# Optimization experiments

Measured on AMD Instinct MI355X. Metric: run time of the kernel, lower is better.

Reference implementation:

```python
import jax, jax.numpy as jnp
import numpy as np

BATCH = 8192
FEATURES = 8192
INITIAL_SPARSITY_RATE = 0.5


def setup_inputs() -> dict:
    key = jax.random.key(0)
    k1, _ = jax.random.split(key)
    inputs = jax.random.normal(k1, (BATCH, FEATURES), dtype=jnp.float32)
    # trainable scalar weight, shape (1,), constant-initialized
    sparsity_rate = jnp.full((1,), INITIAL_SPARSITY_RATE, dtype=jnp.float32)
    return {"inputs": inputs, "sparsity_rate": sparsity_rate}


def reference(inputs, sparsity_rate):
    # inputs: [B, F]; sparsity_rate: [1]
    n = inputs.shape[-1]
    # descending sort along feature axis
    sorted_desc = -jnp.sort(-inputs, axis=-1)
    # per-call threshold index (integer cast, non-differentiable like TF's tf.cast)
    rate = jnp.clip(sparsity_rate[0], 0.0, 1.0)
    idx = jax.lax.stop_gradient((rate * jnp.float32(n)).astype(jnp.int32))
    thresh = jnp.take(sorted_desc, idx, axis=-1)           # [B]: value at rank `idx`
    max_in = jnp.max(inputs, axis=-1)                      # [B]
    t_r = max_in - thresh                                  # [B]
    # relu-masked weights: relu(x + t_r - max) == relu(x - thresh)
    w_t = jax.nn.relu(inputs + t_r[:, None] - max_in[:, None])
    weighted_exp = w_t * jnp.exp(inputs)                   # [B, F]
    sum_we = jnp.sum(weighted_exp, axis=-1, keepdims=True)
    return weighted_exp / sum_we
```

## Files before the change

### kernel.cpp

```cpp
#include <hip/hip_runtime.h>

#define ROWS 8192
#define COLS 8192
#define TPB  256
#define EPT  32
#define VPT  8
#define NW   4

__device__ __forceinline__ unsigned f2k(float x) {
    unsigned u = __float_as_uint(x);
    return (u & 0x80000000u) ? ~u : (u | 0x80000000u);
}
__device__ __forceinline__ float k2f(unsigned k) {
    unsigned u = (k & 0x80000000u) ? (k & 0x7FFFFFFFu) : ~k;
    return __uint_as_float(u);
}

__global__ __launch_bounds__(TPB, 4)
void rsoftmax_kernel(const float* __restrict__ in,
                     const float* __restrict__ rate_p,
                     float* __restrict__ out)
{
    const int t    = threadIdx.x;
    const int lane = t & 63;
    const int wave = t >> 6;
    const int row  = blockIdx.x;
    const float4* in4  = (const float4*)(in  + (size_t)row * COLS);
    float4*       out4 = (float4*)      (out + (size_t)row * COLS);

    unsigned key[EPT];
    #pragma unroll
    for (int j = 0; j < VPT; ++j) {
        float4 v = in4[t + j * TPB];
        key[4*j+0] = f2k(v.x);
        key[4*j+1] = f2k(v.y);
        key[4*j+2] = f2k(v.z);
        key[4*j+3] = f2k(v.w);
    }

    float rate = rate_p[0];
    rate = fminf(fmaxf(rate, 0.0f), 1.0f);
    int idx = (int)(rate * (float)COLS);
    if (idx > COLS - 1) idx = COLS - 1;
    if (idx < 0) idx = 0;

    __shared__ unsigned sHistW[NW][256];
    __shared__ unsigned sWaveTot[NW];
    __shared__ unsigned sK, sPfx;
    __shared__ float    sSum[NW];
    __shared__ float    sInv;

    if (t == 0) { sK = (unsigned)(idx + 1); sPfx = 0u; }

    #pragma unroll
    for (int pass = 0; pass < 4; ++pass) {
        const int      s      = 24 - 8 * pass;
        const unsigned himask = (pass == 0) ? 0u : (0xFFFFFFFFu << (s + 8));

        __syncthreads();
        const unsigned pfx = sPfx;
        const unsigned kk  = sK;

        #pragma unroll
        for (int i = 0; i < 4; ++i) sHistW[wave][lane + 64*i] = 0u;

        #pragma unroll
        for (int j = 0; j < EPT; ++j) {
            if (((key[j] ^ pfx) & himask) == 0u)
                atomicAdd(&sHistW[wave][(key[j] >> s) & 0xFFu], 1u);
        }
        __syncthreads();

        const unsigned h = sHistW[0][t] + sHistW[1][t] + sHistW[2][t] + sHistW[3][t];

        unsigned v = h;
        #pragma unroll
        for (int off = 1; off < 64; off <<= 1) {
            unsigned u = __shfl_down(v, off, 64);
            v += (lane + off < 64) ? u : 0u;
        }
        if (lane == 0) sWaveTot[wave] = v;
        __syncthreads();

        unsigned above = 0u;
        #pragma unroll
        for (int w = 0; w < NW; ++w)
            if (w > wave) above += sWaveTot[w];

        const unsigned st = v + above;
        const unsigned sn = st - h;
        if (st >= kk && sn < kk) {
            sPfx = pfx | ((unsigned)t << s);
            sK   = kk - sn;
        }
    }
    __syncthreads();
    const float thr = k2f(sPfx);

    float wx[EPT];
    float lsum = 0.0f;
    #pragma unroll
    for (int j = 0; j < EPT; ++j) {
        float x = k2f(key[j]);
        float e = fmaxf(x - thr, 0.0f) * __expf(x);
        wx[j] = e;
        lsum += e;
    }
    #pragma unroll
    for (int off = 32; off > 0; off >>= 1)
        lsum += __shfl_down(lsum, off, 64);
    if (lane == 0) sSum[wave] = lsum;
    __syncthreads();
    if (t == 0) sInv = 1.0f / (sSum[0] + sSum[1] + sSum[2] + sSum[3]);
    __syncthreads();
    const float inv = sInv;

    #pragma unroll
    for (int j = 0; j < VPT; ++j) {
        float4 o;
        o.x = wx[4*j+0] * inv;
        o.y = wx[4*j+1] * inv;
        o.z = wx[4*j+2] * inv;
        o.w = wx[4*j+3] * inv;
        out4[t + j * TPB] = o;
    }
}

extern "C" void kernel_launch(void* const* d_in, const int* in_sizes, int n_in,
                              void* d_out, int out_size, void* d_ws, size_t ws_size,
                              hipStream_t stream)
{
    const float* in   = (const float*)d_in[0];
    const float* rate = (const float*)d_in[1];
    float*       out  = (float*)d_out;
    rsoftmax_kernel<<<dim3(ROWS), dim3(TPB), 0, stream>>>(in, rate, out);
}
```

Baseline: 457.4 us.

## Use 512-thread blocks, halve per-thread registers, recompute exp instead of storing

The block doubles to 512 threads with 16 elements each and 8 waves of histogram copies. Only the first 256 threads run the scan and the bucket selection. The weighted exponentials are no longer kept in a register array; they are recomputed in the output pass, and an empty asm pins the keys in VGPRs. Together these cut register pressure so more waves can be resident and hide memory latency. The cost is twice the exp work, two extra histogram merges per pass, and idle threads during the scan.

```diff
diff --git a/kernel.cpp b/kernel.cpp
--- a/kernel.cpp
+++ b/kernel.cpp
@@ -2,10 +2,10 @@
 
 #define ROWS 8192
 #define COLS 8192
-#define TPB  256
-#define EPT  32
-#define VPT  8
-#define NW   4
+#define TPB  512
+#define EPT  16
+#define VPT  4
+#define NW   8
 
 __device__ __forceinline__ unsigned f2k(float x) {
     unsigned u = __float_as_uint(x);
@@ -16,7 +16,7 @@
     return __uint_as_float(u);
 }
 
-__global__ __launch_bounds__(TPB, 4)
+__global__ __launch_bounds__(TPB, 8)
 void rsoftmax_kernel(const float* __restrict__ in,
                      const float* __restrict__ rate_p,
                      float* __restrict__ out)
@@ -37,6 +37,8 @@
         key[4*j+2] = f2k(v.z);
         key[4*j+3] = f2k(v.w);
     }
+    #pragma unroll
+    for (int j = 0; j < EPT; ++j) asm volatile("" : "+v"(key[j]));
 
     float rate = rate_p[0];
     rate = fminf(fmaxf(rate, 0.0f), 1.0f);
@@ -45,7 +47,7 @@
     if (idx < 0) idx = 0;
 
     __shared__ unsigned sHistW[NW][256];
-    __shared__ unsigned sWaveTot[NW];
+    __shared__ unsigned sWaveTot[4];
     __shared__ unsigned sK, sPfx;
     __shared__ float    sSum[NW];
     __shared__ float    sInv;
@@ -71,57 +73,65 @@
         }
         __syncthreads();
 
-        const unsigned h = sHistW[0][t] + sHistW[1][t] + sHistW[2][t] + sHistW[3][t];
+        unsigned h = 0, v = 0;
+        if (t < 256) {
+            #pragma unroll
+            for (int w = 0; w < NW; ++w) h += sHistW[w][t];
 
-        unsigned v = h;
-        #pragma unroll
-        for (int off = 1; off < 64; off <<= 1) {
-            unsigned u = __shfl_down(v, off, 64);
-            v += (lane + off < 64) ? u : 0u;
+            v = h;
+            #pragma unroll
+            for (int off = 1; off < 64; off <<= 1) {
+                unsigned u = __shfl_down(v, off, 64);
+                v += (lane + off < 64) ? u : 0u;
+            }
+            if (lane == 0) sWaveTot[wave] = v;
         }
-        if (lane == 0) sWaveTot[wave] = v;
         __syncthreads();
 
-        unsigned above = 0u;
-        #pragma unroll
-        for (int w = 0; w < NW; ++w)
-            if (w > wave) above += sWaveTot[w];
+        if (t < 256) {
+            unsigned above = 0u;
+            #pragma unroll
+            for (int w = 0; w < 4; ++w)
+                if (w > wave) above += sWaveTot[w];
 
-        const unsigned st = v + above;
-        const unsigned sn = st - h;
-        if (st >= kk && sn < kk) {
-            sPfx = pfx | ((unsigned)t << s);
-            sK   = kk - sn;
+            const unsigned st = v + above;
+            const unsigned sn = st - h;
+            if (st >= kk && sn < kk) {
+                sPfx = pfx | ((unsigned)t << s);
+                sK   = kk - sn;
+            }
         }
     }
     __syncthreads();
     const float thr = k2f(sPfx);
 
-    float wx[EPT];
     float lsum = 0.0f;
     #pragma unroll
     for (int j = 0; j < EPT; ++j) {
         float x = k2f(key[j]);
-        float e = fmaxf(x - thr, 0.0f) * __expf(x);
-        wx[j] = e;
-        lsum += e;
+        lsum += fmaxf(x - thr, 0.0f) * __expf(x);
     }
     #pragma unroll
     for (int off = 32; off > 0; off >>= 1)
         lsum += __shfl_down(lsum, off, 64);
     if (lane == 0) sSum[wave] = lsum;
     __syncthreads();
-    if (t == 0) sInv = 1.0f / (sSum[0] + sSum[1] + sSum[2] + sSum[3]);
+    if (t == 0) {
+        float s = 0.0f;
+        #pragma unroll
+        for (int w = 0; w < NW; ++w) s += sSum[w];
+        sInv = 1.0f / s;
+    }
     __syncthreads();
     const float inv = sInv;
 
     #pragma unroll
     for (int j = 0; j < VPT; ++j) {
         float4 o;
-        o.x = wx[4*j+0] * inv;
-        o.y = wx[4*j+1] * inv;
-        o.z = wx[4*j+2] * inv;
-        o.w = wx[4*j+3] * inv;
+        float x0 = k2f(key[4*j+0]); o.x = fmaxf(x0 - thr, 0.0f) * __expf(x0) * inv;
+        float x1 = k2f(key[4*j+1]); o.y = fmaxf(x1 - thr, 0.0f) * __expf(x1) * inv;
+        float x2 = k2f(key[4*j+2]); o.z = fmaxf(x2 - thr, 0.0f) * __expf(x2) * inv;
+        float x3 = k2f(key[4*j+3]); o.w = fmaxf(x3 - thr, 0.0f) * __expf(x3) * inv;
         out4[t + j * TPB] = o;
     }
 }
```

Result: no change. 464.9 us (+1.6%).
